# Optimization experiments

Measured on AMD Instinct MI355X. Metric: run time of the kernel, lower is better.

Reference implementation:

```python
import jax, jax.numpy as jnp
import numpy as np


def _transmittance(delta_density):
    # exclusive cumulative sum along the sample axis, then exp(-.)
    csum = jnp.cumsum(delta_density[..., :-1, :], axis=-2)
    zeros = jnp.zeros((*csum.shape[:-2], 1, csum.shape[-1]), dtype=delta_density.dtype)
    return jnp.exp(-jnp.concatenate([zeros, csum], axis=-2))


def setup_inputs() -> dict:
    key = jax.random.key(0)
    ks = jax.random.split(key, 6)
    R, S = 16384, 256
    return {
        "object_rgbs": jax.random.uniform(ks[0], (R, S, 3), dtype=jnp.float32),
        "medium_rgbs": jax.random.uniform(ks[1], (R, S, 3), dtype=jnp.float32),
        "direct_coeffs": jax.random.uniform(ks[2], (R, S, 3), dtype=jnp.float32),
        "backscatter_coeffs": jax.random.uniform(ks[3], (R, S, 3), dtype=jnp.float32),
        "densities": jax.random.uniform(ks[4], (R, S, 1), dtype=jnp.float32),
        "deltas": jax.random.uniform(ks[5], (R, S, 1), dtype=jnp.float32) * 0.05,
    }


def reference(object_rgbs, medium_rgbs, direct_coeffs, backscatter_coeffs, densities, deltas):
    object_rgbs = jnp.nan_to_num(object_rgbs)
    medium_rgbs = jnp.nan_to_num(medium_rgbs)
    direct_coeffs = jnp.nan_to_num(direct_coeffs)
    backscatter_coeffs = jnp.nan_to_num(backscatter_coeffs)

    deltas = jax.lax.stop_gradient(deltas)  # ray_samples.deltas.detach()
    delta_densities = deltas * densities                       # [R,S,1]

    object_transmittance = _transmittance(delta_densities)     # [R,S,1]
    object_alphas = 1.0 - jnp.exp(-delta_densities)            # [R,S,1]
    object_weights = object_transmittance * object_alphas      # [R,S,1]

    restored = jnp.clip(jnp.sum(object_weights * object_rgbs, axis=-2), 0.0, 1.0)

    direct_attenuation = _transmittance(direct_coeffs * deltas)             # [R,S,3]
    direct_weights = object_transmittance * direct_attenuation * object_alphas
    direct_ray = jnp.sum(direct_weights * object_rgbs, axis=-2)             # [R,3]
    direct = jnp.clip(direct_ray, 0.0, 1.0)

    bs_dd = backscatter_coeffs * deltas                                     # [R,S,3]
    backscattering = _transmittance(bs_dd)
    medium_alphas = 1.0 - jnp.exp(-bs_dd)
    backscatter_weights = object_transmittance * backscattering * medium_alphas
    backscatter_ray = jnp.sum(backscatter_weights * medium_rgbs, axis=-2)   # [R,3]
    backscatter = jnp.clip(backscatter_ray, 0.0, 1.0)

    rgb = jnp.clip(direct_ray + backscatter_ray, 0.0, 1.0)
    object_mask = jnp.clip(jnp.sum(object_weights, axis=-2), 0.0, 1.0)

    return (rgb, restored, direct, backscatter, object_transmittance,
            object_alphas, object_weights, direct_coeffs[:, 0, :],
            backscatter_coeffs[:, 0, :], object_mask)
```

## Files before the change

### kernel.cpp

```cpp
#include <hip/hip_runtime.h>


#define LOG2E 1.4426950408889634f

__device__ __forceinline__ float clip01(float x) {
    return fminf(fmaxf(x, 0.0f), 1.0f);
}

template <int CTRL, int ROW_MASK, bool BND>
__device__ __forceinline__ float dpp_mov(float v) {
    return __int_as_float(__builtin_amdgcn_update_dpp(
        0, __float_as_int(v), CTRL, ROW_MASK, 0xf, BND));
}

template <int N>
__device__ __forceinline__ void wave_iscan(float (&v)[N]) {
#pragma unroll
    for (int j = 0; j < N; ++j) v[j] += dpp_mov<0x111, 0xf, true>(v[j]);
#pragma unroll
    for (int j = 0; j < N; ++j) v[j] += dpp_mov<0x112, 0xf, true>(v[j]);
#pragma unroll
    for (int j = 0; j < N; ++j) v[j] += dpp_mov<0x114, 0xf, true>(v[j]);
#pragma unroll
    for (int j = 0; j < N; ++j) v[j] += dpp_mov<0x118, 0xf, true>(v[j]);
#pragma unroll
    for (int j = 0; j < N; ++j) v[j] += dpp_mov<0x142, 0xa, false>(v[j]);
#pragma unroll
    for (int j = 0; j < N; ++j) v[j] += dpp_mov<0x143, 0xc, false>(v[j]);
}

__global__ __launch_bounds__(256, 4) void seathru_render(
    const float* __restrict__ g_orgb,
    const float* __restrict__ g_mrgb,
    const float* __restrict__ g_dc,
    const float* __restrict__ g_bc,
    const float* __restrict__ g_den,
    const float* __restrict__ g_del,
    float* __restrict__ out, int R)
{
    const int S = 256;
    const int ray  = blockIdx.x * 4 + (threadIdx.x >> 6);
    const int lane = threadIdx.x & 63;
    if (ray >= R) return;

    const size_t b3 = (size_t)ray * (S * 3);
    const size_t b1 = (size_t)ray * S;
    const size_t RS = (size_t)R * S;

    float4 dl4 = *((const float4*)(g_del + b1) + lane);
    float4 dn4 = *((const float4*)(g_den + b1) + lane);

    float dcv[12], bcv[12], orv[12], mrv[12];
    {
        const float4* p = (const float4*)(g_dc + b3) + lane * 3;
        *(float4*)&dcv[0] = p[0]; *(float4*)&dcv[4] = p[1]; *(float4*)&dcv[8] = p[2];
    }
    {
        const float4* p = (const float4*)(g_bc + b3) + lane * 3;
        *(float4*)&bcv[0] = p[0]; *(float4*)&bcv[4] = p[1]; *(float4*)&bcv[8] = p[2];
    }
    {
        const float4* p = (const float4*)(g_orgb + b3) + lane * 3;
        *(float4*)&orv[0] = p[0]; *(float4*)&orv[4] = p[1]; *(float4*)&orv[8] = p[2];
    }
    {
        const float4* p = (const float4*)(g_mrgb + b3) + lane * 3;
        *(float4*)&mrv[0] = p[0]; *(float4*)&mrv[4] = p[1]; *(float4*)&mrv[8] = p[2];
    }

    const float del[4] = {dl4.x * LOG2E, dl4.y * LOG2E, dl4.z * LOG2E, dl4.w * LOG2E};
    const float den[4] = {dn4.x, dn4.y, dn4.z, dn4.w};

    float dd[4], alpha[4];
#pragma unroll
    for (int i = 0; i < 4; ++i) {
        dd[i]    = del[i] * den[i];
        alpha[i] = 1.0f - exp2f(-dd[i]);
    }

    float aorv[12];
    float mamr[12];
#pragma unroll
    for (int i = 0; i < 4; ++i) {
#pragma unroll
        for (int c = 0; c < 3; ++c) {
            aorv[i * 3 + c] = alpha[i] * orv[i * 3 + c];
            const float bsd = bcv[i * 3 + c] * del[i];
            mamr[i * 3 + c] = (1.0f - exp2f(-bsd)) * mrv[i * 3 + c];
        }
    }

    float ser[7][4];
    float run[7];
#pragma unroll
    for (int q = 0; q < 7; ++q) run[q] = 0.0f;
#pragma unroll
    for (int i = 0; i < 4; ++i) {
        ser[0][i] = run[0]; run[0] += dd[i];
#pragma unroll
        for (int c = 0; c < 3; ++c) {
            ser[1 + c][i] = run[1 + c]; run[1 + c] += dd[i] + dcv[i * 3 + c] * del[i];
            ser[4 + c][i] = run[4 + c]; run[4 + c] += dd[i] + bcv[i * 3 + c] * del[i];
        }
    }

    float sc[7];
#pragma unroll
    for (int q = 0; q < 7; ++q) sc[q] = run[q];
    wave_iscan<7>(sc);
    float off[7];
#pragma unroll
    for (int q = 0; q < 7; ++q) off[q] = sc[q] - run[q];

    float T[4], w[4];
#pragma unroll
    for (int i = 0; i < 4; ++i) {
        T[i] = exp2f(-(off[0] + ser[0][i]));
        w[i] = T[i] * alpha[i];
    }

    float* outT = out + (size_t)12 * R;
    float* outA = outT + RS;
    float* outW = outA + RS;
    {
        float4 t4 = {T[0], T[1], T[2], T[3]};
        float4 a4 = {alpha[0], alpha[1], alpha[2], alpha[3]};
        float4 w4 = {w[0], w[1], w[2], w[3]};
        *((float4*)(outT + b1) + lane) = t4;
        *((float4*)(outA + b1) + lane) = a4;
        *((float4*)(outW + b1) + lane) = w4;
    }

    float acc[10];
#pragma unroll
    for (int c = 0; c < 3; ++c) {
        float ad = 0.0f, ab = 0.0f, ar = 0.0f;
#pragma unroll
        for (int i = 0; i < 4; ++i) {
            ad += exp2f(-(off[1 + c] + ser[1 + c][i])) * aorv[i * 3 + c];
            ab += exp2f(-(off[4 + c] + ser[4 + c][i])) * mamr[i * 3 + c];
            ar += T[i] * aorv[i * 3 + c];
        }
        acc[c]     = ad;
        acc[3 + c] = ab;
        acc[6 + c] = ar;
    }
    acc[9] = w[0] + w[1] + w[2] + w[3];

    wave_iscan<10>(acc);

    if (lane == 63) {
        float* rgb  = out;
        float* rest = out + (size_t)3 * R;
        float* dir  = out + (size_t)6 * R;
        float* bs   = out + (size_t)9 * R;
        float* dc0  = out + (size_t)12 * R + 3 * RS;
        float* bc0  = dc0 + (size_t)3 * R;
        float* mask = bc0 + (size_t)3 * R;
#pragma unroll
        for (int c = 0; c < 3; ++c) {
            const float d = acc[c], b = acc[3 + c];
            rgb[ray * 3 + c]  = clip01(d + b);
            dir[ray * 3 + c]  = clip01(d);
            bs[ray * 3 + c]   = clip01(b);
            rest[ray * 3 + c] = clip01(acc[6 + c]);
        }
        mask[ray] = clip01(acc[9]);
    }
    if (lane == 0) {
        float* dc0 = out + (size_t)12 * R + 3 * RS;
        float* bc0 = dc0 + (size_t)3 * R;
#pragma unroll
        for (int c = 0; c < 3; ++c) {
            dc0[ray * 3 + c] = dcv[c];
            bc0[ray * 3 + c] = bcv[c];
        }
    }
}

extern "C" void kernel_launch(void* const* d_in, const int* in_sizes, int n_in,
                              void* d_out, int out_size, void* d_ws, size_t ws_size,
                              hipStream_t stream) {
    const float* orgb = (const float*)d_in[0];
    const float* mrgb = (const float*)d_in[1];
    const float* dc   = (const float*)d_in[2];
    const float* bc   = (const float*)d_in[3];
    const float* den  = (const float*)d_in[4];
    const float* del  = (const float*)d_in[5];

    const int S = 256;
    const int R = in_sizes[0] / (S * 3);

    dim3 block(256);
    dim3 grid((R + 3) / 4);
    seathru_render<<<grid, block, 0, stream>>>(orgb, mrgb, dc, bc, den, del,
                                               (float*)d_out, R);
}
```

Baseline: 239.6 us.

## Use persistent grid-stride waves with inline-asm batched global loads

Replaces the one-ray-per-wave launch with a persistent grid of 512 blocks that loops over rays with a grid stride. All fourteen vector loads per ray are issued back to back in one inline asm block followed by a single full wait, and the occupancy hint in launch_bounds drops from 4 to 2. The aim is to cut block launch overhead and get many outstanding loads in flight per wave. The fixed grid may leave some compute units underused. The asm block waits for every load before any work starts and leaves no overlap across loop iterations.

```diff
diff --git a/kernel.cpp b/kernel.cpp
--- a/kernel.cpp
+++ b/kernel.cpp
@@ -2,6 +2,8 @@
 
 
 #define LOG2E 1.4426950408889634f
+
+typedef float f4 __attribute__((ext_vector_type(4)));
 
 __device__ __forceinline__ float clip01(float x) {
     return fminf(fmaxf(x, 0.0f), 1.0f);
@@ -29,7 +31,7 @@
     for (int j = 0; j < N; ++j) v[j] += dpp_mov<0x143, 0xc, false>(v[j]);
 }
 
-__global__ __launch_bounds__(256, 4) void seathru_render(
+__global__ __launch_bounds__(256, 2) void seathru_render(
     const float* __restrict__ g_orgb,
     const float* __restrict__ g_mrgb,
     const float* __restrict__ g_dc,
@@ -39,141 +41,167 @@
     float* __restrict__ out, int R)
 {
     const int S = 256;
-    const int ray  = blockIdx.x * 4 + (threadIdx.x >> 6);
-    const int lane = threadIdx.x & 63;
-    if (ray >= R) return;
-
-    const size_t b3 = (size_t)ray * (S * 3);
-    const size_t b1 = (size_t)ray * S;
-    const size_t RS = (size_t)R * S;
-
-    float4 dl4 = *((const float4*)(g_del + b1) + lane);
-    float4 dn4 = *((const float4*)(g_den + b1) + lane);
-
-    float dcv[12], bcv[12], orv[12], mrv[12];
-    {
-        const float4* p = (const float4*)(g_dc + b3) + lane * 3;
-        *(float4*)&dcv[0] = p[0]; *(float4*)&dcv[4] = p[1]; *(float4*)&dcv[8] = p[2];
-    }
-    {
-        const float4* p = (const float4*)(g_bc + b3) + lane * 3;
-        *(float4*)&bcv[0] = p[0]; *(float4*)&bcv[4] = p[1]; *(float4*)&bcv[8] = p[2];
-    }
-    {
-        const float4* p = (const float4*)(g_orgb + b3) + lane * 3;
-        *(float4*)&orv[0] = p[0]; *(float4*)&orv[4] = p[1]; *(float4*)&orv[8] = p[2];
-    }
-    {
-        const float4* p = (const float4*)(g_mrgb + b3) + lane * 3;
-        *(float4*)&mrv[0] = p[0]; *(float4*)&mrv[4] = p[1]; *(float4*)&mrv[8] = p[2];
-    }
-
-    const float del[4] = {dl4.x * LOG2E, dl4.y * LOG2E, dl4.z * LOG2E, dl4.w * LOG2E};
-    const float den[4] = {dn4.x, dn4.y, dn4.z, dn4.w};
-
-    float dd[4], alpha[4];
-#pragma unroll
-    for (int i = 0; i < 4; ++i) {
-        dd[i]    = del[i] * den[i];
-        alpha[i] = 1.0f - exp2f(-dd[i]);
-    }
-
-    float aorv[12];
-    float mamr[12];
-#pragma unroll
-    for (int i = 0; i < 4; ++i) {
-#pragma unroll
-        for (int c = 0; c < 3; ++c) {
-            aorv[i * 3 + c] = alpha[i] * orv[i * 3 + c];
-            const float bsd = bcv[i * 3 + c] * del[i];
-            mamr[i * 3 + c] = (1.0f - exp2f(-bsd)) * mrv[i * 3 + c];
-        }
-    }
-
-    float ser[7][4];
-    float run[7];
-#pragma unroll
-    for (int q = 0; q < 7; ++q) run[q] = 0.0f;
-#pragma unroll
-    for (int i = 0; i < 4; ++i) {
-        ser[0][i] = run[0]; run[0] += dd[i];
-#pragma unroll
-        for (int c = 0; c < 3; ++c) {
-            ser[1 + c][i] = run[1 + c]; run[1 + c] += dd[i] + dcv[i * 3 + c] * del[i];
-            ser[4 + c][i] = run[4 + c]; run[4 + c] += dd[i] + bcv[i * 3 + c] * del[i];
-        }
-    }
-
-    float sc[7];
-#pragma unroll
-    for (int q = 0; q < 7; ++q) sc[q] = run[q];
-    wave_iscan<7>(sc);
-    float off[7];
-#pragma unroll
-    for (int q = 0; q < 7; ++q) off[q] = sc[q] - run[q];
-
-    float T[4], w[4];
-#pragma unroll
-    for (int i = 0; i < 4; ++i) {
-        T[i] = exp2f(-(off[0] + ser[0][i]));
-        w[i] = T[i] * alpha[i];
-    }
+    const int lane   = threadIdx.x & 63;
+    const int wid    = blockIdx.x * 4 + (threadIdx.x >> 6);
+    const int stride = gridDim.x * 4;
+    const size_t RS  = (size_t)R * S;
 
     float* outT = out + (size_t)12 * R;
     float* outA = outT + RS;
     float* outW = outA + RS;
-    {
-        float4 t4 = {T[0], T[1], T[2], T[3]};
-        float4 a4 = {alpha[0], alpha[1], alpha[2], alpha[3]};
-        float4 w4 = {w[0], w[1], w[2], w[3]};
-        *((float4*)(outT + b1) + lane) = t4;
-        *((float4*)(outA + b1) + lane) = a4;
-        *((float4*)(outW + b1) + lane) = w4;
-    }
-
-    float acc[10];
-#pragma unroll
-    for (int c = 0; c < 3; ++c) {
-        float ad = 0.0f, ab = 0.0f, ar = 0.0f;
-#pragma unroll
-        for (int i = 0; i < 4; ++i) {
-            ad += exp2f(-(off[1 + c] + ser[1 + c][i])) * aorv[i * 3 + c];
-            ab += exp2f(-(off[4 + c] + ser[4 + c][i])) * mamr[i * 3 + c];
-            ar += T[i] * aorv[i * 3 + c];
-        }
-        acc[c]     = ad;
-        acc[3 + c] = ab;
-        acc[6 + c] = ar;
-    }
-    acc[9] = w[0] + w[1] + w[2] + w[3];
-
-    wave_iscan<10>(acc);
-
-    if (lane == 63) {
-        float* rgb  = out;
-        float* rest = out + (size_t)3 * R;
-        float* dir  = out + (size_t)6 * R;
-        float* bs   = out + (size_t)9 * R;
-        float* dc0  = out + (size_t)12 * R + 3 * RS;
-        float* bc0  = dc0 + (size_t)3 * R;
-        float* mask = bc0 + (size_t)3 * R;
+
+    for (int ray = wid; ray < R; ray += stride) {
+        const size_t b3 = (size_t)ray * (S * 3);
+        const size_t b1 = (size_t)ray * S;
+
+        const float* p_or = g_orgb + b3 + (size_t)lane * 12;
+        const float* p_dc = g_dc   + b3 + (size_t)lane * 12;
+        const float* p_bc = g_bc   + b3 + (size_t)lane * 12;
+        const float* p_mr = g_mrgb + b3 + (size_t)lane * 12;
+        const float* p_dl = g_del  + b1 + (size_t)lane * 4;
+        const float* p_dn = g_den  + b1 + (size_t)lane * 4;
+
+        f4 orA, orB, orC, dcA, dcB, dcC, bcA, bcB, bcC, mrA, mrB, mrC, dl4, dn4;
+        asm volatile(
+            "global_load_dwordx4 %0,  %14, off\n\t"
+            "global_load_dwordx4 %1,  %14, off offset:16\n\t"
+            "global_load_dwordx4 %2,  %14, off offset:32\n\t"
+            "global_load_dwordx4 %3,  %15, off\n\t"
+            "global_load_dwordx4 %4,  %15, off offset:16\n\t"
+            "global_load_dwordx4 %5,  %15, off offset:32\n\t"
+            "global_load_dwordx4 %6,  %16, off\n\t"
+            "global_load_dwordx4 %7,  %16, off offset:16\n\t"
+            "global_load_dwordx4 %8,  %16, off offset:32\n\t"
+            "global_load_dwordx4 %9,  %17, off\n\t"
+            "global_load_dwordx4 %10, %17, off offset:16\n\t"
+            "global_load_dwordx4 %11, %17, off offset:32\n\t"
+            "global_load_dwordx4 %12, %18, off\n\t"
+            "global_load_dwordx4 %13, %19, off\n\t"
+            "s_waitcnt vmcnt(0)"
+            : "=&v"(orA), "=&v"(orB), "=&v"(orC),
+              "=&v"(dcA), "=&v"(dcB), "=&v"(dcC),
+              "=&v"(bcA), "=&v"(bcB), "=&v"(bcC),
+              "=&v"(mrA), "=&v"(mrB), "=&v"(mrC),
+              "=&v"(dl4), "=&v"(dn4)
+            : "v"(p_or), "v"(p_dc), "v"(p_bc), "v"(p_mr), "v"(p_dl), "v"(p_dn));
+
+        const float dcv[12] = {dcA[0], dcA[1], dcA[2], dcA[3],
+                               dcB[0], dcB[1], dcB[2], dcB[3],
+                               dcC[0], dcC[1], dcC[2], dcC[3]};
+        const float bcv[12] = {bcA[0], bcA[1], bcA[2], bcA[3],
+                               bcB[0], bcB[1], bcB[2], bcB[3],
+                               bcC[0], bcC[1], bcC[2], bcC[3]};
+        const float orv[12] = {orA[0], orA[1], orA[2], orA[3],
+                               orB[0], orB[1], orB[2], orB[3],
+                               orC[0], orC[1], orC[2], orC[3]};
+        const float mrv[12] = {mrA[0], mrA[1], mrA[2], mrA[3],
+                               mrB[0], mrB[1], mrB[2], mrB[3],
+                               mrC[0], mrC[1], mrC[2], mrC[3]};
+
+        const float del[4] = {dl4[0] * LOG2E, dl4[1] * LOG2E,
+                              dl4[2] * LOG2E, dl4[3] * LOG2E};
+        const float den[4] = {dn4[0], dn4[1], dn4[2], dn4[3]};
+
+        float dd[4], alpha[4];
+#pragma unroll
+        for (int i = 0; i < 4; ++i) {
+            dd[i]    = del[i] * den[i];
+            alpha[i] = 1.0f - exp2f(-dd[i]);
+        }
+
+        float aorv[12];
+        float mamr[12];
+#pragma unroll
+        for (int i = 0; i < 4; ++i) {
+#pragma unroll
+            for (int c = 0; c < 3; ++c) {
+                aorv[i * 3 + c] = alpha[i] * orv[i * 3 + c];
+                const float bsd = bcv[i * 3 + c] * del[i];
+                mamr[i * 3 + c] = (1.0f - exp2f(-bsd)) * mrv[i * 3 + c];
+            }
+        }
+
+        float ser[7][4];
+        float run[7];
+#pragma unroll
+        for (int q = 0; q < 7; ++q) run[q] = 0.0f;
+#pragma unroll
+        for (int i = 0; i < 4; ++i) {
+            ser[0][i] = run[0]; run[0] += dd[i];
+#pragma unroll
+            for (int c = 0; c < 3; ++c) {
+                ser[1 + c][i] = run[1 + c]; run[1 + c] += dd[i] + dcv[i * 3 + c] * del[i];
+                ser[4 + c][i] = run[4 + c]; run[4 + c] += dd[i] + bcv[i * 3 + c] * del[i];
+            }
+        }
+
+        float sc[7];
+#pragma unroll
+        for (int q = 0; q < 7; ++q) sc[q] = run[q];
+        wave_iscan<7>(sc);
+        float off[7];
+#pragma unroll
+        for (int q = 0; q < 7; ++q) off[q] = sc[q] - run[q];
+
+        float T[4], w[4];
+#pragma unroll
+        for (int i = 0; i < 4; ++i) {
+            T[i] = exp2f(-(off[0] + ser[0][i]));
+            w[i] = T[i] * alpha[i];
+        }
+        {
+            float4 t4 = {T[0], T[1], T[2], T[3]};
+            float4 a4 = {alpha[0], alpha[1], alpha[2], alpha[3]};
+            float4 w4 = {w[0], w[1], w[2], w[3]};
+            *((float4*)(outT + b1) + lane) = t4;
+            *((float4*)(outA + b1) + lane) = a4;
+            *((float4*)(outW + b1) + lane) = w4;
+        }
+
+        float acc[10];
 #pragma unroll
         for (int c = 0; c < 3; ++c) {
-            const float d = acc[c], b = acc[3 + c];
-            rgb[ray * 3 + c]  = clip01(d + b);
-            dir[ray * 3 + c]  = clip01(d);
-            bs[ray * 3 + c]   = clip01(b);
-            rest[ray * 3 + c] = clip01(acc[6 + c]);
-        }
-        mask[ray] = clip01(acc[9]);
-    }
-    if (lane == 0) {
-        float* dc0 = out + (size_t)12 * R + 3 * RS;
-        float* bc0 = dc0 + (size_t)3 * R;
-#pragma unroll
-        for (int c = 0; c < 3; ++c) {
-            dc0[ray * 3 + c] = dcv[c];
-            bc0[ray * 3 + c] = bcv[c];
+            float ad = 0.0f, ab = 0.0f, ar = 0.0f;
+#pragma unroll
+            for (int i = 0; i < 4; ++i) {
+                ad += exp2f(-(off[1 + c] + ser[1 + c][i])) * aorv[i * 3 + c];
+                ab += exp2f(-(off[4 + c] + ser[4 + c][i])) * mamr[i * 3 + c];
+                ar += T[i] * aorv[i * 3 + c];
+            }
+            acc[c]     = ad;
+            acc[3 + c] = ab;
+            acc[6 + c] = ar;
+        }
+        acc[9] = w[0] + w[1] + w[2] + w[3];
+
+        wave_iscan<10>(acc);
+
+        if (lane == 63) {
+            float* rgb  = out;
+            float* rest = out + (size_t)3 * R;
+            float* dir  = out + (size_t)6 * R;
+            float* bs   = out + (size_t)9 * R;
+            float* dc0  = out + (size_t)12 * R + 3 * RS;
+            float* bc0  = dc0 + (size_t)3 * R;
+            float* mask = bc0 + (size_t)3 * R;
+#pragma unroll
+            for (int c = 0; c < 3; ++c) {
+                const float d = acc[c], b = acc[3 + c];
+                rgb[ray * 3 + c]  = clip01(d + b);
+                dir[ray * 3 + c]  = clip01(d);
+                bs[ray * 3 + c]   = clip01(b);
+                rest[ray * 3 + c] = clip01(acc[6 + c]);
+            }
+            mask[ray] = clip01(acc[9]);
+        }
+        if (lane == 0) {
+            float* dc0 = out + (size_t)12 * R + 3 * RS;
+            float* bc0 = dc0 + (size_t)3 * R;
+#pragma unroll
+            for (int c = 0; c < 3; ++c) {
+                dc0[ray * 3 + c] = dcv[c];
+                bc0[ray * 3 + c] = bcv[c];
+            }
         }
     }
 }
@@ -191,8 +219,12 @@
     const int S = 256;
     const int R = in_sizes[0] / (S * 3);
 
+    int nblk = 512;
+    int need = (R + 3) / 4;
+    if (need < nblk) nblk = need;
+
     dim3 block(256);
-    dim3 grid((R + 3) / 4);
+    dim3 grid(nblk);
     seathru_render<<<grid, block, 0, stream>>>(orgb, mrgb, dc, bc, den, del,
                                                (float*)d_out, R);
 }
```

New measurement: 245.1 us. 2.3% more time.
